# Performance work log

Measured on AMD Instinct MI355X. Metric: run time of the kernel, lower is better.

The kernel has to match this reference:

```python
import jax, jax.numpy as jnp
import numpy as np

DIM_IN, DIM_Q, DIM_V = 1024, 1024, 1024
B, S = 4, 2048
NEG_INF = 1.0e9


def setup_inputs() -> dict:
    key = jax.random.key(0)
    ks = jax.random.split(key, 11)
    c_q = (6.0 / (DIM_IN + DIM_Q)) ** 0.5
    c_v = (6.0 / (DIM_IN + DIM_V)) ** 0.5
    b_bound = 1.0 / np.sqrt(DIM_IN)  # torch Linear default bias init
    return {
        "query": jax.random.normal(ks[0], (B, S, DIM_IN), jnp.float32),
        "key": jax.random.normal(ks[1], (B, S, DIM_IN), jnp.float32),
        "value": jax.random.normal(ks[2], (B, S, DIM_IN), jnp.float32),
        "mask": jax.random.randint(ks[3], (B, S, S), 0, 2).astype(bool),
        "Wq": jax.random.uniform(ks[4], (DIM_Q, DIM_IN), jnp.float32, -c_q, c_q),
        "bq": jax.random.uniform(ks[5], (DIM_Q,), jnp.float32, -b_bound, b_bound),
        "Wk": jax.random.uniform(ks[6], (DIM_Q, DIM_IN), jnp.float32, -c_q, c_q),
        "bk": jax.random.uniform(ks[7], (DIM_Q,), jnp.float32, -b_bound, b_bound),
        "Wv": jax.random.uniform(ks[8], (DIM_V, DIM_IN), jnp.float32, -c_v, c_v),
        "bv": jax.random.uniform(ks[9], (DIM_V,), jnp.float32, -b_bound, b_bound),
    }


def reference(query, key, value, mask, Wq, bq, Wk, bk, Wv, bv):
    q = jnp.einsum("bsd,qd->bsq", query, Wq) + bq  # [B,S,dim_q]
    k = jnp.einsum("bsd,qd->bsq", key, Wk) + bk    # [B,S,dim_q]
    v = jnp.einsum("bsd,vd->bsv", value, Wv) + bv  # [B,S,dim_v]
    scale = 1.0 / jnp.sqrt(jnp.asarray(q.shape[-1], q.dtype))
    scores = jnp.einsum("bqd,bkd->bqk", q, k) * scale  # [B,S,S]
    scores = jnp.where(mask, -NEG_INF, scores)
    affinity = jax.nn.softmax(scores, axis=-1)
    out = jnp.einsum("bqk,bkv->bqv", affinity, v)  # [B,S,dim_v]
    return out
```

## Files before the change

### kernel.cpp

```cpp
#include <hip/hip_runtime.h>

#define BB 4
#define SS 2048
#define DD 1024

typedef __attribute__((ext_vector_type(8))) short short8;
typedef __attribute__((ext_vector_type(4))) float f32x4;

__device__ __forceinline__ unsigned short f2b(float f) {
  unsigned u = __builtin_bit_cast(unsigned, f);
  u += 0x7fffu + ((u >> 16) & 1u);
  return (unsigned short)(u >> 16);
}
__device__ __forceinline__ float b2f(unsigned short us) {
  unsigned u = (unsigned)us << 16;
  return __builtin_bit_cast(float, u);
}

__device__ __forceinline__ void gl2lds16(const void* g, void* l) {
  __builtin_amdgcn_global_load_lds(
      (__attribute__((address_space(1))) unsigned int*)(void*)(size_t)(uintptr_t)g,
      (__attribute__((address_space(3))) unsigned int*)l, 16, 0, 0);
}

__global__ __launch_bounds__(256) void cvt_all(
    const float* __restrict__ q, const float* __restrict__ k, const float* __restrict__ v,
    const float* __restrict__ wq, const float* __restrict__ wk, const float* __restrict__ wv,
    unsigned short* __restrict__ qo, unsigned short* __restrict__ ko, unsigned short* __restrict__ vo,
    unsigned short* __restrict__ wqo, unsigned short* __restrict__ wko, unsigned short* __restrict__ wvo) {
  const int z = blockIdx.z;
  const float* s;
  unsigned short* d;
  size_t i;
  if (blockIdx.x < 4096) {
    s = z == 0 ? q : (z == 1 ? k : v);
    d = z == 0 ? qo : (z == 1 ? ko : vo);
    i = (size_t)blockIdx.x * 2048 + threadIdx.x * 8;
  } else {
    s = z == 0 ? wq : (z == 1 ? wk : wv);
    d = z == 0 ? wqo : (z == 1 ? wko : wvo);
    i = (size_t)(blockIdx.x - 4096) * 2048 + threadIdx.x * 8;
  }
  float4 a = *(const float4*)(s + i);
  float4 b = *(const float4*)(s + i + 4);
  union { unsigned short us[8]; uint4 v4; } o;
  o.us[0] = f2b(a.x); o.us[1] = f2b(a.y); o.us[2] = f2b(a.z); o.us[3] = f2b(a.w);
  o.us[4] = f2b(b.x); o.us[5] = f2b(b.y); o.us[6] = f2b(b.z); o.us[7] = f2b(b.w);
  *(uint4*)(d + i) = o.v4;
}

enum { EPI_BIAS_COL = 0, EPI_BIAS_ROW = 1, EPI_SCORE = 2, EPI_OUT = 3 };

#define BAR() __builtin_amdgcn_s_barrier()
#define LG0() asm volatile("s_waitcnt lgkmcnt(0)")
#define VMW4() asm volatile("s_waitcnt vmcnt(4)")
#define VMW0() asm volatile("s_waitcnt vmcnt(0)")

#define MMA_QUAD(MH, NH)                                                       \
  do {                                                                         \
    __builtin_amdgcn_s_setprio(1);                                             \
    _Pragma("unroll") for (int mt = 0; mt < 4; ++mt)                           \
        _Pragma("unroll") for (int nt = 0; nt < 2; ++nt)                       \
            _Pragma("unroll") for (int ks = 0; ks < 2; ++ks)                   \
                acc[MH][NH][mt][nt] = __builtin_amdgcn_mfma_f32_16x16x32_bf16( \
                    afr[mt][ks], bfr[nt][ks], acc[MH][NH][mt][nt], 0, 0, 0);   \
    __builtin_amdgcn_s_setprio(0);                                             \
  } while (0)

template <int EPI>
__global__ __launch_bounds__(512, 2) void gemm256(
    const unsigned short* __restrict__ A, int lda, long long aBatch,
    const unsigned short* __restrict__ Bm, int ldb, long long bBatch,
    void* __restrict__ Cv, int ldc, long long cBatch, int K,
    const float* __restrict__ bias,
    const float* __restrict__ bias2,
    float scale) {
  __shared__ __attribute__((aligned(1024))) char bA00[16384];
  __shared__ __attribute__((aligned(1024))) char bA01[16384];
  __shared__ __attribute__((aligned(1024))) char bA10[16384];
  __shared__ __attribute__((aligned(1024))) char bA11[16384];
  __shared__ __attribute__((aligned(1024))) char bB00[16384];
  __shared__ __attribute__((aligned(1024))) char bB01[16384];
  __shared__ __attribute__((aligned(1024))) char bB10[16384];
  __shared__ __attribute__((aligned(1024))) char bB11[16384];

  const int tid = threadIdx.x;
  const int wave = tid >> 6, lane = tid & 63;
  const int l15 = lane & 15, quad = lane >> 4;
  const int wr = wave >> 2, wc = wave & 3;
  const int bm = blockIdx.x * 256, bn = blockIdx.y * 256, z = blockIdx.z;
  A += (long long)z * aBatch;
  Bm += (long long)z * bBatch;

  const int laneterm = l15 * 64 + ((quad * 16) ^ ((l15 & 8) << 2));

  size_t aoff0, aoff1, boff0, boff1;
  int dst0, dst1;
  {
    int s = tid, s2 = s ^ (((s >> 5) & 1) << 1);
    int row = (s2 >> 7) * 16 + ((s2 >> 2) & 15);
    int col = ((s2 >> 6) & 1) * 32 + (s2 & 3) * 8;
    aoff0 = (size_t)(bm + row) * lda + col;
    boff0 = (size_t)(bn + row) * ldb + col;
    dst0 = (tid & ~63) * 16;
    s = tid + 512; s2 = s ^ (((s >> 5) & 1) << 1);
    row = (s2 >> 7) * 16 + ((s2 >> 2) & 15);
    col = ((s2 >> 6) & 1) * 32 + (s2 & 3) * 8;
    aoff1 = (size_t)(bm + row) * lda + col;
    boff1 = (size_t)(bn + row) * ldb + col;
    dst1 = dst0 + 8192;
  }

  auto stageA = [&](char* d, int half, int t) {
    const unsigned short* s0 = A + aoff0 + (size_t)(half * 128) * lda + t * 64;
    const unsigned short* s1 = A + aoff1 + (size_t)(half * 128) * lda + t * 64;
    gl2lds16(s0, d + dst0);
    gl2lds16(s1, d + dst1);
  };
  auto stageB = [&](char* d, int half, int t) {
    const unsigned short* s0 = Bm + boff0 + (size_t)(half * 128) * ldb + t * 64;
    const unsigned short* s1 = Bm + boff1 + (size_t)(half * 128) * ldb + t * 64;
    gl2lds16(s0, d + dst0);
    gl2lds16(s1, d + dst1);
  };

  f32x4 acc[2][2][4][2] = {};
  short8 afr[4][2], bfr[2][2];

  auto loadA = [&](const char* rg) {
#pragma unroll
    for (int mt = 0; mt < 4; ++mt)
#pragma unroll
      for (int ks = 0; ks < 2; ++ks)
        afr[mt][ks] = *(const short8*)(rg + ((wr * 4 + mt) * 2 + ks) * 1024 + laneterm);
  };
  auto loadB = [&](const char* rg) {
#pragma unroll
    for (int nt = 0; nt < 2; ++nt)
#pragma unroll
      for (int ks = 0; ks < 2; ++ks)
        bfr[nt][ks] = *(const short8*)(rg + ((wc * 2 + nt) * 2 + ks) * 1024 + laneterm);
  };

  const int NT = K >> 6;
  const int NI = NT >> 1;

  stageA(bA00, 0, 0); stageA(bA01, 1, 0); stageB(bB00, 0, 0); stageB(bB01, 1, 0);
  stageA(bA10, 0, 1); stageB(bB10, 0, 1);
  VMW4(); BAR();

  for (int i = 0; i < NI - 1; ++i) {
    const int t1 = 2 * i + 1;
    loadA(bA00); loadB(bB00); stageA(bA11, 1, t1);          BAR(); LG0(); MMA_QUAD(0, 0); BAR();
    loadB(bB01);              stageB(bB11, 1, t1);          BAR(); LG0(); MMA_QUAD(0, 1); BAR();
    loadA(bA01); loadB(bB00); stageA(bA00, 0, t1 + 1);      BAR(); LG0(); MMA_QUAD(1, 0); BAR();
    loadB(bB01);              stageB(bB00, 0, t1 + 1);
    VMW4();                                                 BAR(); LG0(); MMA_QUAD(1, 1); BAR();
    loadA(bA10); loadB(bB10); stageA(bA01, 1, t1 + 1);      BAR(); LG0(); MMA_QUAD(0, 0); BAR();
    loadB(bB11);              stageB(bB01, 1, t1 + 1);      BAR(); LG0(); MMA_QUAD(0, 1); BAR();
    loadA(bA11); loadB(bB10); stageA(bA10, 0, t1 + 2);      BAR(); LG0(); MMA_QUAD(1, 0); BAR();
    loadB(bB11);              stageB(bB10, 0, t1 + 2);
    VMW4();                                                 BAR(); LG0(); MMA_QUAD(1, 1); BAR();
  }
  {
    const int t1 = NT - 1;
    loadA(bA00); loadB(bB00); stageA(bA11, 1, t1);          BAR(); LG0(); MMA_QUAD(0, 0); BAR();
    loadB(bB01);              stageB(bB11, 1, t1);          BAR(); LG0(); MMA_QUAD(0, 1); BAR();
    loadA(bA01); loadB(bB00);                               BAR(); LG0(); MMA_QUAD(1, 0); BAR();
    loadB(bB01);
    VMW0();                                                 BAR(); LG0(); MMA_QUAD(1, 1); BAR();
    loadA(bA10); loadB(bB10);                               BAR(); LG0(); MMA_QUAD(0, 0); BAR();
    loadB(bB11);                                            BAR(); LG0(); MMA_QUAD(0, 1); BAR();
    loadA(bA11); loadB(bB10);                               BAR(); LG0(); MMA_QUAD(1, 0); BAR();
    loadB(bB11);                                            BAR(); LG0(); MMA_QUAD(1, 1);
  }

  const int r0 = bm + wr * 64 + quad * 4;
  const int c0 = bn + wc * 32 + l15;
  if constexpr (EPI == EPI_SCORE) {
    unsigned short* Cz = (unsigned short*)Cv + (long long)z * cBatch;
#pragma unroll
    for (int mh = 0; mh < 2; ++mh)
#pragma unroll
      for (int mt = 0; mt < 4; ++mt)
#pragma unroll
        for (int r = 0; r < 4; ++r) {
          const int row = r0 + mh * 128 + mt * 16 + r;
#pragma unroll
          for (int nh = 0; nh < 2; ++nh)
#pragma unroll
            for (int nt = 0; nt < 2; ++nt)
              Cz[(size_t)row * ldc + c0 + nh * 128 + nt * 16] =
                  f2b(acc[mh][nh][mt][nt][r] * scale);
        }
  } else if constexpr (EPI == EPI_OUT) {
    float* Cz = (float*)Cv + (long long)z * cBatch;
#pragma unroll
    for (int mh = 0; mh < 2; ++mh)
#pragma unroll
      for (int mt = 0; mt < 4; ++mt)
#pragma unroll
        for (int r = 0; r < 4; ++r) {
          const int row = r0 + mh * 128 + mt * 16 + r;
#pragma unroll
          for (int nh = 0; nh < 2; ++nh)
#pragma unroll
            for (int nt = 0; nt < 2; ++nt)
              Cz[(size_t)row * ldc + c0 + nh * 128 + nt * 16] = acc[mh][nh][mt][nt][r];
        }
  } else {
    const float* bp = (z == 0) ? bias : bias2;
    unsigned short* Cz = (unsigned short*)Cv + (long long)z * cBatch;
#pragma unroll
    for (int mh = 0; mh < 2; ++mh)
#pragma unroll
      for (int mt = 0; mt < 4; ++mt)
#pragma unroll
        for (int r = 0; r < 4; ++r) {
          const int row = r0 + mh * 128 + mt * 16 + r;
#pragma unroll
          for (int nh = 0; nh < 2; ++nh)
#pragma unroll
            for (int nt = 0; nt < 2; ++nt) {
              const int col = c0 + nh * 128 + nt * 16;
              float v = acc[mh][nh][mt][nt][r] +
                        (EPI == EPI_BIAS_COL ? bp[col] : bp[row]);
              Cz[(size_t)row * ldc + col] = f2b(v);
            }
        }
  }
}

__global__ __launch_bounds__(256) void softmax_rows(const unsigned short* __restrict__ Sc,
                                                    const void* __restrict__ mask,
                                                    unsigned short* __restrict__ P) {
  const size_t r = blockIdx.x;
  const unsigned short* src = Sc + r * SS;
  unsigned short* dst = P + r * SS;
  const int tid = threadIdx.x;
  const int wave = tid >> 6, lane = tid & 63;
  __shared__ int anyv[4];
  __shared__ float red[8];

  unsigned pw = ((const unsigned*)mask)[tid];
  unsigned long long bal = __ballot(pw > 1u);
  if (lane == 0) anyv[wave] = (bal != 0ULL) ? 1 : 0;
  __syncthreads();
  const bool isU8 = (anyv[0] | anyv[1] | anyv[2] | anyv[3]) != 0;

  unsigned mbits = 0;
  if (isU8) {
    uint2 v = *(const uint2*)((const unsigned char*)mask + r * SS + tid * 8);
#pragma unroll
    for (int j = 0; j < 4; ++j) {
      mbits |= (((v.x >> (8 * j)) & 0xffu) ? 1u : 0u) << j;
      mbits |= (((v.y >> (8 * j)) & 0xffu) ? 1u : 0u) << (j + 4);
    }
  } else {
    const uint4* p = (const uint4*)((const int*)mask + r * SS + tid * 8);
    uint4 a = p[0], b = p[1];
    mbits = (a.x ? 1u : 0u) | ((a.y ? 1u : 0u) << 1) | ((a.z ? 1u : 0u) << 2) |
            ((a.w ? 1u : 0u) << 3) | ((b.x ? 1u : 0u) << 4) | ((b.y ? 1u : 0u) << 5) |
            ((b.z ? 1u : 0u) << 6) | ((b.w ? 1u : 0u) << 7);
  }

  union { unsigned short us[8]; uint4 v; } in;
  in.v = *(const uint4*)(src + tid * 8);
  float xs[8];
#pragma unroll
  for (int k = 0; k < 8; ++k)
    xs[k] = ((mbits >> k) & 1u) ? -1.0e9f : b2f(in.us[k]);
  float mx = xs[0];
#pragma unroll
  for (int k = 1; k < 8; ++k) mx = fmaxf(mx, xs[k]);
#pragma unroll
  for (int o = 32; o; o >>= 1) mx = fmaxf(mx, __shfl_xor(mx, o));
  if (lane == 0) red[wave] = mx;
  __syncthreads();
  mx = fmaxf(fmaxf(red[0], red[1]), fmaxf(red[2], red[3]));
  float e[8], s = 0.f;
#pragma unroll
  for (int k = 0; k < 8; ++k) { e[k] = __expf(xs[k] - mx); s += e[k]; }
#pragma unroll
  for (int o = 32; o; o >>= 1) s += __shfl_xor(s, o);
  if (lane == 0) red[4 + wave] = s;
  __syncthreads();
  s = (red[4] + red[5]) + (red[6] + red[7]);
  float inv = 1.0f / s;
  union { unsigned short us[8]; uint4 v; } o;
#pragma unroll
  for (int k = 0; k < 8; ++k) o.us[k] = f2b(e[k] * inv);
  *(uint4*)(dst + tid * 8) = o.v;
}

extern "C" void kernel_launch(void* const* d_in, const int* in_sizes, int n_in,
                              void* d_out, int out_size, void* d_ws, size_t ws_size,
                              hipStream_t stream) {
  const float* query = (const float*)d_in[0];
  const float* key   = (const float*)d_in[1];
  const float* value = (const float*)d_in[2];
  const void*  mask  = d_in[3];
  const float* Wq = (const float*)d_in[4];
  const float* bq = (const float*)d_in[5];
  const float* Wk = (const float*)d_in[6];
  const float* bk = (const float*)d_in[7];
  const float* Wv = (const float*)d_in[8];
  const float* bv = (const float*)d_in[9];
  float* out = (float*)d_out;

  char* ws = (char*)d_ws;
  const size_t MB = 1024 * 1024;
  unsigned short* qin = (unsigned short*)(ws + 0 * MB);
  unsigned short* kin = (unsigned short*)(ws + 16 * MB);
  unsigned short* vin = (unsigned short*)(ws + 32 * MB);
  unsigned short* Wqb = (unsigned short*)(ws + 48 * MB);
  unsigned short* Wkb = (unsigned short*)(ws + 50 * MB);
  unsigned short* Wvb = (unsigned short*)(ws + 52 * MB);
  unsigned short* qb  = (unsigned short*)(ws + 54 * MB);
  unsigned short* kb  = (unsigned short*)(ws + 70 * MB);
  unsigned short* vT  = (unsigned short*)(ws + 86 * MB);
  unsigned short* Sc  = (unsigned short*)(ws + 102 * MB);
  unsigned short* P   = (unsigned short*)(ws + 134 * MB);

  dim3 blk(256), blk512(512);

  cvt_all<<<dim3(4608, 1, 3), blk, 0, stream>>>(
      query, key, value, Wq, Wk, Wv, qin, kin, vin, Wqb, Wkb, Wvb);

  gemm256<EPI_BIAS_COL><<<dim3(32, 4, 2), blk512, 0, stream>>>(
      qin, 1024, 8388608LL, Wqb, 1024, 1048576LL, qb, 1024, 8388608LL,
      1024, bq, bk, 0.f);

  gemm256<EPI_BIAS_ROW><<<dim3(4, 32, 1), blk512, 0, stream>>>(
      Wvb, 1024, 0, vin, 1024, 0, vT, 8192, 0, 1024, bv, bv, 0.f);

  gemm256<EPI_SCORE><<<dim3(8, 8, BB), blk512, 0, stream>>>(
      qb, 1024, (long long)SS * 1024, kb, 1024, (long long)SS * 1024,
      Sc, SS, (long long)SS * SS, 1024, nullptr, nullptr, 0.03125f);

  softmax_rows<<<dim3(BB * SS), blk, 0, stream>>>(Sc, mask, P);

  gemm256<EPI_OUT><<<dim3(8, 4, BB), blk512, 0, stream>>>(
      P, SS, (long long)SS * SS, vT, 8192, (long long)SS,
      out, 1024, (long long)SS * 1024, SS, nullptr, nullptr, 1.f);
}
```

Baseline: 388.7 us.

## Double-buffer LDS fragments and deepen global-to-LDS prefetch in GEMM main loop

Restructures the 256x256 bf16 GEMM main loop so register fragments are double-buffered (fa0/fa1, fb0/fb1). The next fragment's LDS read and the next global-to-LDS stage are issued before the current MFMA block runs, and there is one barrier per step instead of two plus explicit lgkmcnt waits. The prologue now preloads a full extra k-tile, and vmcnt waits become finer grained (10, then a graded drain in the tail). Address offsets also move to 32-bit ints. The aim is to overlap LDS and global latency with MFMA work. The cost is more VGPRs for the duplicated fragments and a risk of hazards in the tighter buffer reuse, which relies on the compiler's implicit lgkmcnt waits.

```diff
diff --git a/kernel.cpp b/kernel.cpp
--- a/kernel.cpp
+++ b/kernel.cpp
@@ -52,18 +52,21 @@
 enum { EPI_BIAS_COL = 0, EPI_BIAS_ROW = 1, EPI_SCORE = 2, EPI_OUT = 3 };
 
 #define BAR() __builtin_amdgcn_s_barrier()
-#define LG0() asm volatile("s_waitcnt lgkmcnt(0)")
+#define VMW10() asm volatile("s_waitcnt vmcnt(10)")
+#define VMW8() asm volatile("s_waitcnt vmcnt(8)")
+#define VMW6() asm volatile("s_waitcnt vmcnt(6)")
 #define VMW4() asm volatile("s_waitcnt vmcnt(4)")
+#define VMW2() asm volatile("s_waitcnt vmcnt(2)")
 #define VMW0() asm volatile("s_waitcnt vmcnt(0)")
 
-#define MMA_QUAD(MH, NH)                                                       \
+#define MMA(FA, FB, MH, NH)                                                    \
   do {                                                                         \
     __builtin_amdgcn_s_setprio(1);                                             \
     _Pragma("unroll") for (int mt = 0; mt < 4; ++mt)                           \
         _Pragma("unroll") for (int nt = 0; nt < 2; ++nt)                       \
             _Pragma("unroll") for (int ks = 0; ks < 2; ++ks)                   \
                 acc[MH][NH][mt][nt] = __builtin_amdgcn_mfma_f32_16x16x32_bf16( \
-                    afr[mt][ks], bfr[nt][ks], acc[MH][NH][mt][nt], 0, 0, 0);   \
+                    FA[mt][ks], FB[nt][ks], acc[MH][NH][mt][nt], 0, 0, 0);     \
     __builtin_amdgcn_s_setprio(0);                                             \
   } while (0)
 
@@ -94,85 +97,82 @@
 
   const int laneterm = l15 * 64 + ((quad * 16) ^ ((l15 & 8) << 2));
 
-  size_t aoff0, aoff1, boff0, boff1;
+  int avoff0, avoff1, bvoff0, bvoff1;
   int dst0, dst1;
   {
     int s = tid, s2 = s ^ (((s >> 5) & 1) << 1);
     int row = (s2 >> 7) * 16 + ((s2 >> 2) & 15);
     int col = ((s2 >> 6) & 1) * 32 + (s2 & 3) * 8;
-    aoff0 = (size_t)(bm + row) * lda + col;
-    boff0 = (size_t)(bn + row) * ldb + col;
+    avoff0 = (bm + row) * lda + col;
+    bvoff0 = (bn + row) * ldb + col;
     dst0 = (tid & ~63) * 16;
     s = tid + 512; s2 = s ^ (((s >> 5) & 1) << 1);
     row = (s2 >> 7) * 16 + ((s2 >> 2) & 15);
     col = ((s2 >> 6) & 1) * 32 + (s2 & 3) * 8;
-    aoff1 = (size_t)(bm + row) * lda + col;
-    boff1 = (size_t)(bn + row) * ldb + col;
+    avoff1 = (bm + row) * lda + col;
+    bvoff1 = (bn + row) * ldb + col;
     dst1 = dst0 + 8192;
   }
 
   auto stageA = [&](char* d, int half, int t) {
-    const unsigned short* s0 = A + aoff0 + (size_t)(half * 128) * lda + t * 64;
-    const unsigned short* s1 = A + aoff1 + (size_t)(half * 128) * lda + t * 64;
-    gl2lds16(s0, d + dst0);
-    gl2lds16(s1, d + dst1);
+    const unsigned short* base = A + (size_t)(half * 128) * lda + (size_t)t * 64;
+    gl2lds16(base + avoff0, d + dst0);
+    gl2lds16(base + avoff1, d + dst1);
   };
   auto stageB = [&](char* d, int half, int t) {
-    const unsigned short* s0 = Bm + boff0 + (size_t)(half * 128) * ldb + t * 64;
-    const unsigned short* s1 = Bm + boff1 + (size_t)(half * 128) * ldb + t * 64;
-    gl2lds16(s0, d + dst0);
-    gl2lds16(s1, d + dst1);
+    const unsigned short* base = Bm + (size_t)(half * 128) * ldb + (size_t)t * 64;
+    gl2lds16(base + bvoff0, d + dst0);
+    gl2lds16(base + bvoff1, d + dst1);
   };
 
   f32x4 acc[2][2][4][2] = {};
-  short8 afr[4][2], bfr[2][2];
-
-  auto loadA = [&](const char* rg) {
+  short8 fa0[4][2], fa1[4][2];
+  short8 fb0[2][2], fb1[2][2];
+
+  auto loadA = [&](const char* rg, short8 (&f)[4][2]) {
 #pragma unroll
     for (int mt = 0; mt < 4; ++mt)
 #pragma unroll
       for (int ks = 0; ks < 2; ++ks)
-        afr[mt][ks] = *(const short8*)(rg + ((wr * 4 + mt) * 2 + ks) * 1024 + laneterm);
+        f[mt][ks] = *(const short8*)(rg + ((wr * 4 + mt) * 2 + ks) * 1024 + laneterm);
   };
-  auto loadB = [&](const char* rg) {
+  auto loadB = [&](const char* rg, short8 (&f)[2][2]) {
 #pragma unroll
     for (int nt = 0; nt < 2; ++nt)
 #pragma unroll
       for (int ks = 0; ks < 2; ++ks)
-        bfr[nt][ks] = *(const short8*)(rg + ((wc * 2 + nt) * 2 + ks) * 1024 + laneterm);
+        f[nt][ks] = *(const short8*)(rg + ((wc * 2 + nt) * 2 + ks) * 1024 + laneterm);
   };
 
   const int NT = K >> 6;
   const int NI = NT >> 1;
 
-  stageA(bA00, 0, 0); stageA(bA01, 1, 0); stageB(bB00, 0, 0); stageB(bB01, 1, 0);
-  stageA(bA10, 0, 1); stageB(bB10, 0, 1);
-  VMW4(); BAR();
+  stageA(bA00, 0, 0); stageB(bB00, 0, 0); stageB(bB01, 1, 0); stageA(bA01, 1, 0);
+  stageA(bA10, 0, 1); stageB(bB10, 0, 1); stageB(bB11, 1, 1); stageA(bA11, 1, 1);
+  VMW8();
+  BAR();
+  loadA(bA00, fa0); loadB(bB00, fb0);
 
   for (int i = 0; i < NI - 1; ++i) {
-    const int t1 = 2 * i + 1;
-    loadA(bA00); loadB(bB00); stageA(bA11, 1, t1);          BAR(); LG0(); MMA_QUAD(0, 0); BAR();
-    loadB(bB01);              stageB(bB11, 1, t1);          BAR(); LG0(); MMA_QUAD(0, 1); BAR();
-    loadA(bA01); loadB(bB00); stageA(bA00, 0, t1 + 1);      BAR(); LG0(); MMA_QUAD(1, 0); BAR();
-    loadB(bB01);              stageB(bB00, 0, t1 + 1);
-    VMW4();                                                 BAR(); LG0(); MMA_QUAD(1, 1); BAR();
-    loadA(bA10); loadB(bB10); stageA(bA01, 1, t1 + 1);      BAR(); LG0(); MMA_QUAD(0, 0); BAR();
-    loadB(bB11);              stageB(bB01, 1, t1 + 1);      BAR(); LG0(); MMA_QUAD(0, 1); BAR();
-    loadA(bA11); loadB(bB10); stageA(bA10, 0, t1 + 2);      BAR(); LG0(); MMA_QUAD(1, 0); BAR();
-    loadB(bB11);              stageB(bB10, 0, t1 + 2);
-    VMW4();                                                 BAR(); LG0(); MMA_QUAD(1, 1); BAR();
+    const int t2 = 2 * i + 2, t3 = 2 * i + 3;
+    loadB(bB01, fb1); stageA(bA00, 0, t2); MMA(fa0, fb0, 0, 0); VMW10(); BAR();
+    loadA(bA01, fa1); stageB(bB00, 0, t2); MMA(fa0, fb1, 0, 1); VMW10(); BAR();
+    loadA(bA10, fa0); stageB(bB01, 1, t2); MMA(fa1, fb0, 1, 0); VMW10(); BAR();
+    loadB(bB10, fb0); stageA(bA01, 1, t2); MMA(fa1, fb1, 1, 1); VMW10(); BAR();
+    loadB(bB11, fb1); stageA(bA10, 0, t3); MMA(fa0, fb0, 0, 0); VMW10(); BAR();
+    loadA(bA11, fa1); stageB(bB10, 0, t3); MMA(fa0, fb1, 0, 1); VMW10(); BAR();
+    loadA(bA00, fa0); stageB(bB11, 1, t3); MMA(fa1, fb0, 1, 0); VMW10(); BAR();
+    loadB(bB00, fb0); stageA(bA11, 1, t3); MMA(fa1, fb1, 1, 1); VMW10(); BAR();
   }
   {
-    const int t1 = NT - 1;
-    loadA(bA00); loadB(bB00); stageA(bA11, 1, t1);          BAR(); LG0(); MMA_QUAD(0, 0); BAR();
-    loadB(bB01);              stageB(bB11, 1, t1);          BAR(); LG0(); MMA_QUAD(0, 1); BAR();
-    loadA(bA01); loadB(bB00);                               BAR(); LG0(); MMA_QUAD(1, 0); BAR();
-    loadB(bB01);
-    VMW0();                                                 BAR(); LG0(); MMA_QUAD(1, 1); BAR();
-    loadA(bA10); loadB(bB10);                               BAR(); LG0(); MMA_QUAD(0, 0); BAR();
-    loadB(bB11);                                            BAR(); LG0(); MMA_QUAD(0, 1); BAR();
-    loadA(bA11); loadB(bB10);                               BAR(); LG0(); MMA_QUAD(1, 0); BAR();
-    loadB(bB11);                                            BAR(); LG0(); MMA_QUAD(1, 1);
+    loadB(bB01, fb1); MMA(fa0, fb0, 0, 0); VMW8(); BAR();
+    loadA(bA01, fa1); MMA(fa0, fb1, 0, 1); VMW6(); BAR();
+    loadA(bA10, fa0); MMA(fa1, fb0, 1, 0); VMW4(); BAR();
+    loadB(bB10, fb0); MMA(fa1, fb1, 1, 1); VMW2(); BAR();
+    loadB(bB11, fb1); MMA(fa0, fb0, 0, 0); VMW0(); BAR();
+    loadA(bA11, fa1); MMA(fa0, fb1, 0, 1); BAR();
+    MMA(fa1, fb0, 1, 0);
+    MMA(fa1, fb1, 1, 1);
   }
 
   const int r0 = bm + wr * 64 + quad * 4;
```

Result: slower. 506.6 us (+30.3%).
